# Optimization experiments

Hardware: AMD Instinct MI355X
Metric: run time of the kernel (lower is better)

## Reference

```python
import jax, jax.numpy as jnp
import numpy as np

N_PATCH = 8      # patch_num = [8, 8]
N_BINS = 256     # histogram bins 0..255


def setup_inputs() -> dict:
    key = jax.random.key(0)
    k1, k2 = jax.random.split(key)
    sr = jax.random.uniform(k1, (16, 3, 1024, 1024), dtype=jnp.float32)
    hr = jax.random.uniform(k2, (16, 3, 1024, 1024), dtype=jnp.float32)
    return {"sr": sr, "hr": hr}


def _entropy_weight(hr):
    """Per-spatial-patch Shannon entropy of 8-bit histogram, broadcast to an
    [H, W] weight map, normalized as (w - w.min()) / w.max() (original w.max,
    matching torch evaluation order)."""
    B, C, H, W = hr.shape
    ph, pw = H // N_PATCH, W // N_PATCH
    # [64, B*C*ph*pw] — each patch covers the full batch+channel slice,
    # exactly as split_patch's img[..., i*ph:(i+1)*ph, j*pw:(j+1)*pw].
    patches = (hr.reshape(B, C, N_PATCH, ph, N_PATCH, pw)
                 .transpose(2, 4, 0, 1, 3, 5)
                 .reshape(N_PATCH * N_PATCH, -1))
    # (patch * 255).int() truncation; values in [0,1) -> bins 0..255
    vals = jnp.clip((patches * 255.0).astype(jnp.int32), 0, N_BINS - 1)
    counts = jax.vmap(lambda v: jnp.bincount(v, length=N_BINS))(vals)
    p = counts.astype(jnp.float32) / jnp.float32(vals.shape[1])  # density (unit bin width)
    safe_p = jnp.where(p > 0, p, 1.0)
    ent = -jnp.sum(jnp.where(p > 0, p * jnp.log2(safe_p), 0.0), axis=1)  # [64]
    # tile each patch's scalar entropy over its spatial block (row-major patch order)
    w = jnp.broadcast_to(ent.reshape(N_PATCH, 1, N_PATCH, 1),
                         (N_PATCH, ph, N_PATCH, pw)).reshape(H, W)
    w = (w - w.min()) / w.max()
    return w  # [H, W], broadcasts over B, C


def reference(sr, hr):
    w = _entropy_weight(hr)
    # L1 loss (mean reduction) on entropy-weighted images
    return jnp.mean(jnp.abs(w * sr - w * hr))
```

## Files before the change

### kernel.cpp

```cpp
#include <hip/hip_runtime.h>
#include <math.h>

#define NP      8
#define NBINS   256
#define BC      48
#define HH      1024
#define WW      1024
#define RPB     16
#define THREADS 256
#define NBLK1   3072
#define BLK_PER_I 384
#define PATCH_ELEMS (BC * 128 * 128)
#define N_TOTAL ((long long)BC * HH * WW)

#define GH_BYTES   ((size_t)NBLK1 * 2048 * 2)
#define GS_OFF     GH_BYTES
#define GS_BYTES   ((size_t)NBLK1 * NP * 4)
#define ENT_OFF    (GS_OFF + GS_BYTES)
#define ENT_BYTES  (64 * 8)
#define GT_OFF     (ENT_OFF + ENT_BYTES)
#define PATHA_BYTES (GT_OFF + 64 * 4)
#define B_GHIST_BYTES (64 * NBINS * 4)
#define B_GSUM_OFF    B_GHIST_BYTES
#define B_ENT_OFF     (B_GSUM_OFF + 256)

__device__ __forceinline__ void load_g(const float4* __restrict__ s4,
                                       const float4* __restrict__ h4,
                                       int g, float4* sb, float4* hb)
{
#pragma unroll
    for (int k = 0; k < 2; ++k) {
        sb[k] = s4[(g * 2 + k) * (WW / 4)];
        hb[k] = h4[(g * 2 + k) * (WW / 4)];
    }
}

__device__ __forceinline__ void proc_g(const float4* sb, const float4* hb,
                                       float& acc, unsigned int* histj)
{
#pragma unroll
    for (int k = 0; k < 2; ++k) {
        float4 s = sb[k], h = hb[k];
        acc += fabsf(s.x - h.x);
        acc += fabsf(s.y - h.y);
        acc += fabsf(s.z - h.z);
        acc += fabsf(s.w - h.w);
        int b0 = min(max((int)(h.x * 255.0f), 0), 255);
        int b1 = min(max((int)(h.y * 255.0f), 0), 255);
        int b2 = min(max((int)(h.z * 255.0f), 0), 255);
        int b3 = min(max((int)(h.w * 255.0f), 0), 255);
        atomicAdd(&histj[b0], 1u);
        atomicAdd(&histj[b1], 1u);
        atomicAdd(&histj[b2], 1u);
        atomicAdd(&histj[b3], 1u);
    }
}

template <bool ATOMIC>
__global__ __launch_bounds__(THREADS, 8)
void entrop_pass1(const float* __restrict__ sr, const float* __restrict__ hr,
                  unsigned int* __restrict__ gh32, float* __restrict__ gs)
{
    __shared__ unsigned int hist[NP * NBINS];
    const int t = threadIdx.x;
#pragma unroll
    for (int m = t; m < NP * NBINS; m += THREADS) hist[m] = 0;
    __syncthreads();

    const int r0 = blockIdx.x * RPB;
    const int i  = (r0 & (HH - 1)) >> 7;
    const int j  = t >> 5;
    unsigned int* histj = &hist[j << 8];

    const float4* s4 = (const float4*)sr + (size_t)r0 * (WW / 4) + t;
    const float4* h4 = (const float4*)hr + (size_t)r0 * (WW / 4) + t;

    float acc = 0.0f;
    float4 sA[2], hA[2], sB[2], hB[2];
    load_g(s4, h4, 0, sA, hA);
#pragma unroll
    for (int g = 0; g < 7; ++g) {
        if (g & 1) { load_g(s4, h4, g + 1, sA, hA); proc_g(sB, hB, acc, histj); }
        else       { load_g(s4, h4, g + 1, sB, hB); proc_g(sA, hA, acc, histj); }
    }
    proc_g(sB, hB, acc, histj);

    for (int off = 16; off; off >>= 1) acc += __shfl_down(acc, off, 32);
    if ((t & 31) == 0) {
        if (ATOMIC) atomicAdd(&gs[i * NP + j], acc);
        else        gs[blockIdx.x * NP + j] = acc;
    }

    __syncthreads();
    if (ATOMIC) {
        for (int m = t; m < NP * NBINS; m += THREADS) {
            unsigned int c = hist[m];
            if (c) atomicAdd(&gh32[i * NP * NBINS + m], c);
        }
    } else {
#pragma unroll
        for (int m = t; m < NP * NBINS / 2; m += THREADS)
            gh32[(size_t)blockIdx.x * (NP * NBINS / 2) + m] =
                hist[2 * m] | (hist[2 * m + 1] << 16);
    }
}

__global__ __launch_bounds__(THREADS)
void entrop_reduceA(const unsigned short* __restrict__ gh,
                    const float* __restrict__ gs,
                    double* __restrict__ ent, float* __restrict__ gsumT)
{
    const int p = blockIdx.x, i = p >> 3, jj = p & 7;
    const int t = threadIdx.x;

    unsigned int cnt = 0;
    const unsigned short* col = gh + jj * NBINS + t;
    for (int g = 0; g < BLK_PER_I / 8; ++g) {
#pragma unroll
        for (int d = 0; d < 8; ++d)
            cnt += col[(size_t)(64 * g + 8 * i + d) * 2048];
    }
    double term = 0.0;
    if (cnt) {
        double pd = (double)cnt * (1.0 / (double)PATCH_ELEMS);
        term = pd * log2(pd);
    }
    float sg = 0.0f;
    for (int idx = t; idx < BLK_PER_I; idx += THREADS) {
        int g = idx >> 3, d = idx & 7;
        sg += gs[(size_t)(64 * g + 8 * i + d) * NP + jj];
    }

    for (int off = 32; off; off >>= 1) {
        term += __shfl_down(term, off, 64);
        sg   += __shfl_down(sg, off, 64);
    }
    __shared__ double rd[4];
    __shared__ float  rf[4];
    if ((t & 63) == 0) { rd[t >> 6] = term; rf[t >> 6] = sg; }
    __syncthreads();
    if (t == 0) {
        ent[p]   = -(rd[0] + rd[1] + rd[2] + rd[3]);
        gsumT[p] = rf[0] + rf[1] + rf[2] + rf[3];
    }
}

__global__ __launch_bounds__(THREADS)
void entrop_reduceB(const unsigned int* __restrict__ ghist, double* __restrict__ ent)
{
    const int p = blockIdx.x, t = threadIdx.x;
    unsigned int c = ghist[p * NBINS + t];
    double term = 0.0;
    if (c) {
        double pd = (double)c * (1.0 / (double)PATCH_ELEMS);
        term = pd * log2(pd);
    }
    for (int off = 32; off; off >>= 1) term += __shfl_down(term, off, 64);
    __shared__ double rd[4];
    if ((t & 63) == 0) rd[t >> 6] = term;
    __syncthreads();
    if (t == 0) ent[p] = -(rd[0] + rd[1] + rd[2] + rd[3]);
}

__global__ void entrop_final(const double* __restrict__ ent,
                             const float* __restrict__ gsumT,
                             float* __restrict__ out)
{
    const int t = threadIdx.x;
    double e = ent[t];
    double mn = e, mx = e;
#pragma unroll
    for (int off = 32; off; off >>= 1) {
        mn = fmin(mn, __shfl_xor(mn, off, 64));
        mx = fmax(mx, __shfl_xor(mx, off, 64));
    }
    double contrib = (e - mn) / mx * (double)gsumT[t];
#pragma unroll
    for (int off = 32; off; off >>= 1) contrib += __shfl_xor(contrib, off, 64);
    if (t == 0) out[0] = (float)(contrib / (double)N_TOTAL);
}

extern "C" void kernel_launch(void* const* d_in, const int* in_sizes, int n_in,
                              void* d_out, int out_size, void* d_ws, size_t ws_size,
                              hipStream_t stream)
{
    const float* sr = (const float*)d_in[0];
    const float* hr = (const float*)d_in[1];
    float* out = (float*)d_out;
    char* ws = (char*)d_ws;

    if (ws_size >= PATHA_BYTES) {
        unsigned int*   gh32  = (unsigned int*)ws;
        float*          gs    = (float*)(ws + GS_OFF);
        double*         ent   = (double*)(ws + ENT_OFF);
        float*          gsumT = (float*)(ws + GT_OFF);
        entrop_pass1<false><<<NBLK1, THREADS, 0, stream>>>(sr, hr, gh32, gs);
        entrop_reduceA<<<64, THREADS, 0, stream>>>((const unsigned short*)gh32, gs, ent, gsumT);
        entrop_final<<<1, 64, 0, stream>>>(ent, gsumT, out);
    } else {
        unsigned int* ghist = (unsigned int*)ws;
        float*        gsum  = (float*)(ws + B_GSUM_OFF);
        double*       ent   = (double*)(ws + B_ENT_OFF);
        hipMemsetAsync(ws, 0, B_GSUM_OFF + 256, stream);
        entrop_pass1<true><<<NBLK1, THREADS, 0, stream>>>(sr, hr, ghist, gsum);
        entrop_reduceB<<<64, THREADS, 0, stream>>>(ghist, ent);
        entrop_final<<<1, 64, 0, stream>>>(ent, gsum, out);
    }
}
```

Before: 404.7 us.

## Double rows per block and prefetch eight rows per group in histogram pass

Each pass-1 block now processes 32 rows instead of 16, halving the block count. It issues eight row loads up front, before the shared histogram is zeroed, and then software-pipelines loading of the next eight-row group against histogram processing of the current one. The occupancy hint drops from 8 to 4 blocks per CU to leave room for the larger register buffers. The reduction kernel's indexing is updated to match the new per-block partial layout; the aim is fewer partial histograms and more memory-level parallelism, at the cost of lower occupancy.

```diff
diff --git a/kernel.cpp b/kernel.cpp
--- a/kernel.cpp
+++ b/kernel.cpp
@@ -6,10 +6,11 @@
 #define BC      48
 #define HH      1024
 #define WW      1024
-#define RPB     16
+#define RPB     32
 #define THREADS 256
-#define NBLK1   3072
-#define BLK_PER_I 384
+#define NBLK1   1536
+#define BLK_PER_I 192
+#define PD      8
 #define PATCH_ELEMS (BC * 128 * 128)
 #define N_TOTAL ((long long)BC * HH * WW)
 
@@ -24,66 +25,65 @@
 #define B_GSUM_OFF    B_GHIST_BYTES
 #define B_ENT_OFF     (B_GSUM_OFF + 256)
 
-__device__ __forceinline__ void load_g(const float4* __restrict__ s4,
-                                       const float4* __restrict__ h4,
-                                       int g, float4* sb, float4* hb)
-{
-#pragma unroll
-    for (int k = 0; k < 2; ++k) {
-        sb[k] = s4[(g * 2 + k) * (WW / 4)];
-        hb[k] = h4[(g * 2 + k) * (WW / 4)];
-    }
-}
-
-__device__ __forceinline__ void proc_g(const float4* sb, const float4* hb,
-                                       float& acc, unsigned int* histj)
-{
-#pragma unroll
-    for (int k = 0; k < 2; ++k) {
-        float4 s = sb[k], h = hb[k];
-        acc += fabsf(s.x - h.x);
-        acc += fabsf(s.y - h.y);
-        acc += fabsf(s.z - h.z);
-        acc += fabsf(s.w - h.w);
-        int b0 = min(max((int)(h.x * 255.0f), 0), 255);
-        int b1 = min(max((int)(h.y * 255.0f), 0), 255);
-        int b2 = min(max((int)(h.z * 255.0f), 0), 255);
-        int b3 = min(max((int)(h.w * 255.0f), 0), 255);
-        atomicAdd(&histj[b0], 1u);
-        atomicAdd(&histj[b1], 1u);
-        atomicAdd(&histj[b2], 1u);
-        atomicAdd(&histj[b3], 1u);
-    }
+__device__ __forceinline__ void proc1(const float4 s, const float4 h,
+                                      float& acc, unsigned int* histj)
+{
+    acc += fabsf(s.x - h.x);
+    acc += fabsf(s.y - h.y);
+    acc += fabsf(s.z - h.z);
+    acc += fabsf(s.w - h.w);
+    int b0 = min(max((int)(h.x * 255.0f), 0), 255);
+    int b1 = min(max((int)(h.y * 255.0f), 0), 255);
+    int b2 = min(max((int)(h.z * 255.0f), 0), 255);
+    int b3 = min(max((int)(h.w * 255.0f), 0), 255);
+    atomicAdd(&histj[b0], 1u);
+    atomicAdd(&histj[b1], 1u);
+    atomicAdd(&histj[b2], 1u);
+    atomicAdd(&histj[b3], 1u);
 }
 
 template <bool ATOMIC>
-__global__ __launch_bounds__(THREADS, 8)
+__global__ __launch_bounds__(THREADS, 4)
 void entrop_pass1(const float* __restrict__ sr, const float* __restrict__ hr,
                   unsigned int* __restrict__ gh32, float* __restrict__ gs)
 {
     __shared__ unsigned int hist[NP * NBINS];
-    const int t = threadIdx.x;
-#pragma unroll
-    for (int m = t; m < NP * NBINS; m += THREADS) hist[m] = 0;
-    __syncthreads();
-
+    const int t  = threadIdx.x;
     const int r0 = blockIdx.x * RPB;
-    const int i  = (r0 & (HH - 1)) >> 7;
-    const int j  = t >> 5;
-    unsigned int* histj = &hist[j << 8];
 
     const float4* s4 = (const float4*)sr + (size_t)r0 * (WW / 4) + t;
     const float4* h4 = (const float4*)hr + (size_t)r0 * (WW / 4) + t;
 
+    float4 sb[PD], hb[PD];
+#pragma unroll
+    for (int k = 0; k < PD; ++k) {
+        sb[k] = s4[k * (WW / 4)];
+        hb[k] = h4[k * (WW / 4)];
+    }
+
+#pragma unroll
+    for (int m = t; m < NP * NBINS; m += THREADS) hist[m] = 0;
+    __syncthreads();
+
+    const int i = (r0 & (HH - 1)) >> 7;
+    const int j = t >> 5;
+    unsigned int* histj = &hist[j << 8];
+
     float acc = 0.0f;
-    float4 sA[2], hA[2], sB[2], hB[2];
-    load_g(s4, h4, 0, sA, hA);
-#pragma unroll
-    for (int g = 0; g < 7; ++g) {
-        if (g & 1) { load_g(s4, h4, g + 1, sA, hA); proc_g(sB, hB, acc, histj); }
-        else       { load_g(s4, h4, g + 1, sB, hB); proc_g(sA, hA, acc, histj); }
-    }
-    proc_g(sB, hB, acc, histj);
+#pragma unroll 1
+    for (int grp = 0; grp < RPB / PD - 1; ++grp) {
+        const float4* sn = s4 + (size_t)(grp + 1) * PD * (WW / 4);
+        const float4* hn = h4 + (size_t)(grp + 1) * PD * (WW / 4);
+#pragma unroll
+        for (int k = 0; k < PD; ++k) {
+            float4 s = sb[k], h = hb[k];
+            sb[k] = sn[k * (WW / 4)];
+            hb[k] = hn[k * (WW / 4)];
+            proc1(s, h, acc, histj);
+        }
+    }
+#pragma unroll
+    for (int k = 0; k < PD; ++k) proc1(sb[k], hb[k], acc, histj);
 
     for (int off = 16; off; off >>= 1) acc += __shfl_down(acc, off, 32);
     if ((t & 31) == 0) {
@@ -115,20 +115,24 @@
 
     unsigned int cnt = 0;
     const unsigned short* col = gh + jj * NBINS + t;
-    for (int g = 0; g < BLK_PER_I / 8; ++g) {
-#pragma unroll
-        for (int d = 0; d < 8; ++d)
-            cnt += col[(size_t)(64 * g + 8 * i + d) * 2048];
+#pragma unroll 1
+    for (int u = 0; u < 48; u += 2) {
+#pragma unroll
+        for (int v = 0; v < 2; ++v)
+#pragma unroll
+            for (int e = 0; e < 4; ++e)
+                cnt += col[(size_t)(32 * (u + v) + 4 * i + e) * 2048];
     }
     double term = 0.0;
     if (cnt) {
         double pd = (double)cnt * (1.0 / (double)PATCH_ELEMS);
         term = pd * log2(pd);
     }
+
     float sg = 0.0f;
-    for (int idx = t; idx < BLK_PER_I; idx += THREADS) {
-        int g = idx >> 3, d = idx & 7;
-        sg += gs[(size_t)(64 * g + 8 * i + d) * NP + jj];
+    if (t < BLK_PER_I) {
+        int u = t >> 2, e = t & 3;
+        sg = gs[(size_t)(32 * u + 4 * i + e) * NP + jj];
     }
 
     for (int off = 32; off; off >>= 1) {
```

New measurement: 414.8 us. 1.02x slower.
